# Optimization experiments

Measured on AMD Instinct MI355X. Metric: run time of the kernel, lower is better.

Reference implementation:

```python
import jax, jax.numpy as jnp
import numpy as np
from jax import lax


def setup_inputs() -> dict:
    key = jax.random.key(0)
    ks = jax.random.split(key, 3)
    N, Cin, Cout, H, W = 4, 256, 256, 96, 96
    x = jax.random.normal(ks[0], (N, Cin, H, W), jnp.float32)
    # DCNv2-style internal offset/mask conv: 27 = 9 dy + 9 dx + 9 mask logits
    w_off = jax.random.normal(ks[1], (27, Cin, 3, 3), jnp.float32) * 0.01
    b_off = jnp.zeros((27,), jnp.float32)
    w = jax.random.normal(ks[2], (Cout, Cin, 3, 3), jnp.float32) * (1.0 / np.sqrt(Cin * 9))
    b = jnp.zeros((Cout,), jnp.float32)
    gamma = jnp.ones((Cout,), jnp.float32)
    beta = jnp.zeros((Cout,), jnp.float32)
    return {"x": x, "w_off": w_off, "b_off": b_off, "w": w, "b": b, "gamma": gamma, "beta": beta}


def _bilinear(img, py, px):
    # img: [C,H,W]; py,px: [K,H,W] float sampling coords. Zero outside bounds.
    C, H, W = img.shape
    flat = img.reshape(C, -1)
    y0 = jnp.floor(py)
    x0 = jnp.floor(px)
    ly = py - y0
    lx = px - x0

    def gather(yc, xc):
        valid = (yc >= 0) & (yc <= H - 1) & (xc >= 0) & (xc <= W - 1)
        yi = jnp.clip(yc, 0, H - 1).astype(jnp.int32)
        xi = jnp.clip(xc, 0, W - 1).astype(jnp.int32)
        idx = (yi * W + xi).reshape(-1)
        v = flat[:, idx].reshape((C,) + yc.shape)  # [C,K,H,W]
        return v * valid.astype(img.dtype)

    v00 = gather(y0, x0)
    v01 = gather(y0, x0 + 1)
    v10 = gather(y0 + 1, x0)
    v11 = gather(y0 + 1, x0 + 1)
    return (v00 * (1 - ly) * (1 - lx) + v01 * (1 - ly) * lx
            + v10 * ly * (1 - lx) + v11 * ly * lx)


def _forward(x, w_off, b_off, w, b, gamma, beta):
    N, C, H, W = x.shape
    Cout = w.shape[0]
    dn = ("NCHW", "OIHW", "NCHW")
    # internal offset/mask conv (3x3, stride 1, pad 1)
    om = lax.conv_general_dilated(x, w_off, (1, 1), [(1, 1), (1, 1)], dimension_numbers=dn)
    om = om + b_off[None, :, None, None]
    dy, dx, m = om[:, :9], om[:, 9:18], jax.nn.sigmoid(om[:, 18:])
    # base 3x3 kernel grid, dilation 1, padding 1 (centered taps -1..1)
    ky, kx = jnp.meshgrid(jnp.arange(3) - 1, jnp.arange(3) - 1, indexing="ij")
    py = dy + jnp.arange(H, dtype=x.dtype)[None, None, :, None] + ky.reshape(1, 9, 1, 1).astype(x.dtype)
    px = dx + jnp.arange(W, dtype=x.dtype)[None, None, None, :] + kx.reshape(1, 9, 1, 1).astype(x.dtype)
    sampled = jax.vmap(_bilinear)(x, py, px)  # [N,C,9,H,W]
    sampled = sampled * m[:, None]            # DCNv2 modulation mask
    y = jnp.einsum("nckhw,ock->nohw", sampled, w.reshape(Cout, C, 9))
    y = y + b[None, :, None, None]
    # BatchNorm2d (training-mode batch statistics) + ReLU
    mean = y.mean(axis=(0, 2, 3))
    var = y.var(axis=(0, 2, 3))
    y = (y - mean[None, :, None, None]) * lax.rsqrt(var[None, :, None, None] + 1e-5)
    y = y * gamma[None, :, None, None] + beta[None, :, None, None]
    return jax.nn.relu(y)


def reference(x, w_off, b_off, w, b, gamma, beta):
    return _forward(x, w_off, b_off, w, b, gamma, beta)
```

## Files before the change

kernel.cpp:

```cpp
#include <hip/hip_runtime.h>
#include <cmath>

#define H 96
#define W 96
#define HW 9216
#define CIN 256
#define COUT 256
#define NB 4
#define NCH 72
#define NGR 36
#define NIV 18

typedef float f32x4 __attribute__((ext_vector_type(4)));
typedef float f32x2 __attribute__((ext_vector_type(2)));
typedef short bf16x8 __attribute__((ext_vector_type(8)));

__device__ __forceinline__ unsigned short f2bf(float f) {
  unsigned int u = __float_as_uint(f);
  u += 0x7fff + ((u >> 16) & 1);
  return (unsigned short)(u >> 16);
}
__device__ __forceinline__ float bf2f(unsigned short u) {
  return __uint_as_float(((unsigned int)u) << 16);
}
__device__ __forceinline__ f32x2 up2(unsigned int u) {
  f32x2 r;
  r.x = __uint_as_float(u << 16);
  r.y = __uint_as_float(u & 0xffff0000u);
  return r;
}
__device__ __forceinline__ unsigned int cvtpk(float lo, float hi) {
  unsigned int r;
  asm("v_cvt_pk_bf16_f32 %0, %1, %2" : "=v"(r) : "v"(lo), "v"(hi));
  return r;
}

__device__ __forceinline__ void bar() {
  asm volatile("s_waitcnt lgkmcnt(0)" ::: "memory");
  __builtin_amdgcn_s_barrier();
  asm volatile("" ::: "memory");
}

__global__ __launch_bounds__(256)
void xt_convert(const float* __restrict__ x, unsigned short* __restrict__ xT) {
  __shared__ unsigned short ls[64][72];
  int tid = threadIdx.x;
  int hwbase = blockIdx.x * 64;
  int cbase  = blockIdx.y * 64;
  int n      = blockIdx.z;

  {
    int cl = tid >> 2, qd = tid & 3;
    const float* src = x + ((size_t)(n * CIN + cbase + cl)) * HW + hwbase + qd * 16;
#pragma unroll
    for (int m = 0; m < 4; ++m) {
      float4 v = *(const float4*)(src + m * 4);
      int hwl = qd * 16 + m * 4;
      ls[hwl + 0][cl] = f2bf(v.x);
      ls[hwl + 1][cl] = f2bf(v.y);
      ls[hwl + 2][cl] = f2bf(v.z);
      ls[hwl + 3][cl] = f2bf(v.w);
    }
  }
  __syncthreads();
  {
    int hw = tid >> 2, part = tid & 3;
    unsigned short* dst = xT + ((size_t)(n * HW + hwbase + hw)) * CIN + cbase + part * 16;
    *(uint4*)(dst + 0) = *(const uint4*)(&ls[hw][part * 16 + 0]);
    *(uint4*)(dst + 8) = *(const uint4*)(&ls[hw][part * 16 + 8]);
  }
}

__global__ __launch_bounds__(256)
void wa_all(const float* __restrict__ w, const float* __restrict__ w_off,
            unsigned short* __restrict__ Ag, unsigned short* __restrict__ Ag2,
            float* __restrict__ sumArr) {
  int bx = blockIdx.x;
  int tid = threadIdx.x;
  if (bx < 288) {
    int gid = bx * 256 + tid;
    int ch = gid >> 10;
    int rest = gid & 1023;
    int ot = rest >> 6, l = rest & 63;
    int o = ot * 16 + (l & 15);
    int k = ch >> 3, cc = ch & 7;
    int cbase = cc * 32 + (l >> 4) * 8;
    unsigned short r[8];
#pragma unroll
    for (int j = 0; j < 8; ++j)
      r[j] = f2bf(w[((size_t)o * CIN + cbase + j) * 9 + k]);
    uint4 pk;
    pk.x = (unsigned int)r[0] | ((unsigned int)r[1] << 16);
    pk.y = (unsigned int)r[2] | ((unsigned int)r[3] << 16);
    pk.z = (unsigned int)r[4] | ((unsigned int)r[5] << 16);
    pk.w = (unsigned int)r[6] | ((unsigned int)r[7] << 16);
    *(uint4*)(Ag + (size_t)gid * 8) = pk;
  } else if (bx < 324) {
    int gid = (bx - 288) * 256 + tid;
    int ch = gid >> 7;
    int rest = gid & 127;
    int ot = rest >> 6, l = rest & 63;
    int o = ot * 16 + (l & 15);
    int k = ch >> 3, cc = ch & 7;
    int cbase = cc * 32 + (l >> 4) * 8;
    unsigned short r[8];
#pragma unroll
    for (int j = 0; j < 8; ++j)
      r[j] = (o < 27) ? f2bf(w_off[((size_t)o * CIN + cbase + j) * 9 + k]) : (unsigned short)0;
    uint4 pk;
    pk.x = (unsigned int)r[0] | ((unsigned int)r[1] << 16);
    pk.y = (unsigned int)r[2] | ((unsigned int)r[3] << 16);
    pk.z = (unsigned int)r[4] | ((unsigned int)r[5] << 16);
    pk.w = (unsigned int)r[6] | ((unsigned int)r[7] << 16);
    *(uint4*)(Ag2 + (size_t)gid * 8) = pk;
  } else {
    sumArr[tid] = 0.f;
    sumArr[256 + tid] = 0.f;
  }
}

__global__ __launch_bounds__(512, 4)
void merged_gemm(const unsigned short* __restrict__ xT,
                 const unsigned short* __restrict__ Ag,
                 const unsigned short* __restrict__ Ag2,
                 const float* __restrict__ b_off,
                 unsigned short* __restrict__ yb,
                 float* __restrict__ sumArr, float* __restrict__ sqArr) {
  __shared__ int   sPos[9][64];
  __shared__ float pymk[27][64];
  __shared__ int   sIdx4[9][64][4];
  __shared__ float sWgt4[9][64][4];
  __shared__ unsigned short sB[2][2][4096];

  int tid = threadIdx.x;
  int wv = tid >> 6, lane = tid & 63, quad = lane >> 4, l16 = lane & 15;
  int pixBase = blockIdx.x * 64;
  int n = blockIdx.y;
  const unsigned short* xTn = xT + (size_t)n * HW * CIN;

  if (tid < 64) {
    int hwp = pixBase + tid;
    int hh = hwp / W, wx = hwp % W;
#pragma unroll
    for (int ty = 0; ty < 3; ++ty) {
#pragma unroll
      for (int tx = 0; tx < 3; ++tx) {
        int iy = hh + ty - 1, ix = wx + tx - 1;
        bool ok = (iy >= 0) && (iy < H) && (ix >= 0) && (ix < W);
        sPos[ty * 3 + tx][tid] = ok ? (iy * W + ix) : -1;
      }
    }
  }
  bar();

  int pixA = tid >> 3, ckA = tid & 7;
  int aA = (ckA >> 2) * 2048 + (pixA >> 4) * 512 + ((ckA & 3) * 16 + ((pixA & 15) ^ (ckA & 3))) * 8;

  f32x4 accA[2];
  accA[0] = (f32x4){0.f, 0.f, 0.f, 0.f};
  accA[1] = (f32x4){0.f, 0.f, 0.f, 0.f};

  uint4 dA, dB;
  auto issueA = [&](int g, uint4* d) {
    int k = g % 9, c2 = g / 9;
    int p = sPos[k][pixA];
    *d = (uint4){0, 0, 0, 0};
    if (p >= 0) *d = *(const uint4*)(xTn + (size_t)p * CIN + c2 * 64 + ckA * 8);
  };

  bf16x8 afrA[4];
  auto aloadA = [&](int g) {
    int k = g % 9, c2 = g / 9;
    int ch = k * 8 + c2 * 2;
#pragma unroll
    for (int s = 0; s < 2; ++s)
#pragma unroll
      for (int ot = 0; ot < 2; ++ot)
        afrA[s * 2 + ot] = *(const bf16x8*)(Ag2 + ((size_t)((ch + s) * 2 + ot) * 64 + lane) * 8);
  };

  int rdA = wv * 512 + (quad * 16 + (l16 ^ quad)) * 8;
  auto mfmaA = [&](int buf, int half) {
    const unsigned short* base = &sB[buf][half][0];
    __builtin_amdgcn_s_setprio(1);
#pragma unroll
    for (int s = 0; s < 2; ++s) {
      bf16x8 bfr = *(const bf16x8*)(base + s * 2048 + rdA);
      accA[0] = __builtin_amdgcn_mfma_f32_16x16x32_bf16(afrA[s * 2 + 0], bfr, accA[0], 0, 0, 0);
      accA[1] = __builtin_amdgcn_mfma_f32_16x16x32_bf16(afrA[s * 2 + 1], bfr, accA[1], 0, 0, 0);
    }
    __builtin_amdgcn_s_setprio(0);
  };
  auto storeA = [&](uint4 d, int buf, int half) {
    *(uint4*)(&sB[buf][half][aA]) = d;
  };

  issueA(0, &dA);
  issueA(1, &dB);
  if (wv < 4) aloadA(0);
  storeA(dA, 0, 0);
  issueA(2, &dA);
  storeA(dB, 0, 1);
  issueA(3, &dB);
  bar();

  for (int i = 0; i < NIV; ++i) {
    int buf = i & 1;
    if (wv < 4) {
      mfmaA(buf, 0);
      aloadA(2 * i + 1);
    }
    if (i < NIV - 1) storeA(dA, buf ^ 1, 0);
    if (i < NIV - 2) issueA(2 * i + 4, &dA);
    if (wv < 4) mfmaA(buf, 1);
    if (i < NIV - 1) storeA(dB, buf ^ 1, 1);
    if (i < NIV - 2) issueA(2 * i + 5, &dB);
    if (i < NIV - 1 && wv < 4) aloadA(2 * i + 2);
    bar();
  }

  if (wv < 4) {
    int pixL = wv * 16 + l16;
    int pixG = pixBase + pixL;
    int he = pixG / W, we = pixG % W;
#pragma unroll
    for (int ot = 0; ot < 2; ++ot) {
#pragma unroll
      for (int r = 0; r < 4; ++r) {
        int kk = ot * 16 + quad * 4 + r;
        if (kk >= 27) continue;
        float v = accA[ot][r] + b_off[kk];
        if (kk < 9) {
          pymk[kk][pixL] = v + (float)he + (float)(kk / 3 - 1);
        } else if (kk < 18) {
          int j = kk - 9;
          pymk[kk][pixL] = v + (float)we + (float)(j % 3 - 1);
        } else {
          pymk[kk][pixL] = 1.f / (1.f + expf(-v));
        }
      }
    }
  }
  bar();

  {
    int pix0 = tid & 63;
    int k0 = tid >> 6;
#pragma unroll
    for (int rep = 0; rep < 2; ++rep) {
      int k = (rep == 0) ? k0 : 8;
      if (rep == 1 && tid >= 64) break;
      float fy = pymk[k][pix0], fx = pymk[9 + k][pix0], fm = pymk[18 + k][pix0];
      float y0f = floorf(fy), x0f = floorf(fx);
      float ly = fy - y0f, lx = fx - x0f;
      int y0 = (int)y0f, x0 = (int)x0f;
      int cy0 = min(max(y0, 0), H - 1), cy1 = min(max(y0 + 1, 0), H - 1);
      int cx0 = min(max(x0, 0), W - 1), cx1 = min(max(x0 + 1, 0), W - 1);
      float vy0 = (y0 >= 0 && y0 <= H - 1) ? 1.f : 0.f;
      float vy1 = (y0 + 1 >= 0 && y0 + 1 <= H - 1) ? 1.f : 0.f;
      float vx0 = (x0 >= 0 && x0 <= W - 1) ? 1.f : 0.f;
      float vx1 = (x0 + 1 >= 0 && x0 + 1 <= W - 1) ? 1.f : 0.f;
      int4 iv;
      iv.x = cy0 * W + cx0;
      iv.y = cy0 * W + cx1;
      iv.z = cy1 * W + cx0;
      iv.w = cy1 * W + cx1;
      float4 wf;
      wf.x = (1.f - ly) * (1.f - lx) * fm * vy0 * vx0;
      wf.y = (1.f - ly) * lx * fm * vy0 * vx1;
      wf.z = ly * (1.f - lx) * fm * vy1 * vx0;
      wf.w = ly * lx * fm * vy1 * vx1;
      *(int4*)(&sIdx4[k][pix0][0]) = iv;
      *(float4*)(&sWgt4[k][pix0][0]) = wf;
    }
  }
  bar();

  int pixS  = ((wv & 3) << 4) | (lane >> 2);
  int qS    = lane & 3;
  int chunk = ((wv >> 2) << 2) | qS;
  int co    = chunk * 8;
  int sAddr = (chunk >> 2) * 2048 + (wv & 3) * 512 + (qS * 16 + ((lane >> 2) ^ qS)) * 8;

  f32x4 acc[2][4];
#pragma unroll
  for (int i = 0; i < 2; ++i)
#pragma unroll
    for (int pt = 0; pt < 4; ++pt) acc[i][pt] = (f32x4){0.f, 0.f, 0.f, 0.f};

  uint4 cnA[4], cnB[4];
  float wgA[4], wgB[4];
  auto issue = [&](int g, uint4* cn, float* wt) {
    int k = g % 9, c2 = g / 9;
    int4 iv = *(const int4*)(&sIdx4[k][pixS][0]);
    float4 wf = *(const float4*)(&sWgt4[k][pixS][0]);
    int coff = c2 * 64 + co;
    cn[0] = *(const uint4*)(xTn + (size_t)iv.x * CIN + coff);
    cn[1] = *(const uint4*)(xTn + (size_t)iv.y * CIN + coff);
    cn[2] = *(const uint4*)(xTn + (size_t)iv.z * CIN + coff);
    cn[3] = *(const uint4*)(xTn + (size_t)iv.w * CIN + coff);
    wt[0] = wf.x; wt[1] = wf.y; wt[2] = wf.z; wt[3] = wf.w;
  };

  auto blendOne = [&](unsigned int u0, unsigned int u1, unsigned int u2,
                      unsigned int u3, const float* wt) -> unsigned int {
    f32x2 s = up2(u0) * wt[0];
    s += up2(u1) * wt[1];
    s += up2(u2) * wt[2];
    s += up2(u3) * wt[3];
    return cvtpk(s.x, s.y);
  };
  auto blendStore = [&](uint4* cn, const float* wt, int buf, int half) {
    uint4 r;
    r.x = blendOne(cn[0].x, cn[1].x, cn[2].x, cn[3].x, wt);
    r.y = blendOne(cn[0].y, cn[1].y, cn[2].y, cn[3].y, wt);
    r.z = blendOne(cn[0].z, cn[1].z, cn[2].z, cn[3].z, wt);
    r.w = blendOne(cn[0].w, cn[1].w, cn[2].w, cn[3].w, wt);
    *(uint4*)(&sB[buf][half][sAddr]) = r;
  };

  bf16x8 afr[4];
  auto aload = [&](int g) {
    int k = g % 9, c2 = g / 9;
    int ch = k * 8 + c2 * 2;
#pragma unroll
    for (int s = 0; s < 2; ++s)
#pragma unroll
      for (int ot = 0; ot < 2; ++ot)
        afr[s * 2 + ot] = *(const bf16x8*)(Ag + ((size_t)((ch + s) * 16 + 2 * wv + ot) * 64 + lane) * 8);
  };

  int rdBase = (quad * 16 + (l16 ^ quad)) * 8;
  auto mfmaPhase = [&](int buf, int half) {
    const unsigned short* base = &sB[buf][half][0];
    __builtin_amdgcn_s_setprio(1);
#pragma unroll
    for (int s = 0; s < 2; ++s) {
      bf16x8 bfr[4];
#pragma unroll
      for (int pt = 0; pt < 4; ++pt)
        bfr[pt] = *(const bf16x8*)(base + s * 2048 + pt * 512 + rdBase);
#pragma unroll
      for (int pt = 0; pt < 4; ++pt) {
        acc[0][pt] = __builtin_amdgcn_mfma_f32_16x16x32_bf16(afr[s * 2 + 0], bfr[pt], acc[0][pt], 0, 0, 0);
        acc[1][pt] = __builtin_amdgcn_mfma_f32_16x16x32_bf16(afr[s * 2 + 1], bfr[pt], acc[1][pt], 0, 0, 0);
      }
    }
    __builtin_amdgcn_s_setprio(0);
  };

  issue(0, cnA, wgA);
  issue(1, cnB, wgB);
  aload(0);
  blendStore(cnA, wgA, 0, 0);
  issue(2, cnA, wgA);
  blendStore(cnB, wgB, 0, 1);
  issue(3, cnB, wgB);
  bar();

  for (int i = 0; i < NIV; ++i) {
    int buf = i & 1;
    mfmaPhase(buf, 0);
    aload(2 * i + 1);
    if (i < NIV - 1) blendStore(cnA, wgA, buf ^ 1, 0);
    if (i < NIV - 2) issue(2 * i + 4, cnA, wgA);
    mfmaPhase(buf, 1);
    if (i < NIV - 1) blendStore(cnB, wgB, buf ^ 1, 1);
    if (i < NIV - 2) issue(2 * i + 5, cnB, wgB);
    if (i < NIV - 1) aload(2 * i + 2);
    bar();
  }

#pragma unroll
  for (int ot = 0; ot < 2; ++ot) {
#pragma unroll
    for (int r = 0; r < 4; ++r) {
      int o = (2 * wv + ot) * 16 + quad * 4 + r;
      unsigned short* rowp = yb + (size_t)(n * COUT + o) * HW + pixBase;
      float s = 0.f, q = 0.f;
#pragma unroll
      for (int pt = 0; pt < 4; ++pt) {
        float v = acc[ot][pt][r];
        rowp[pt * 16 + l16] = f2bf(v);
        s += v;
        q = fmaf(v, v, q);
      }
#pragma unroll
      for (int m = 8; m >= 1; m >>= 1) {
        s += __shfl_xor(s, m, 64);
        q += __shfl_xor(q, m, 64);
      }
      if (l16 == 0) {
        atomicAdd(&sumArr[o], s);
        atomicAdd(&sqArr[o], q);
      }
    }
  }
}

__global__ __launch_bounds__(256)
void bn_apply(const unsigned short* __restrict__ yb,
              float* __restrict__ out,
              const float* __restrict__ sumArr,
              const float* __restrict__ sqArr,
              const float* __restrict__ gamma,
              const float* __restrict__ beta) {
  int gid = blockIdx.x * 256 + threadIdx.x;
  int base = gid * 8;
  int o = (base / HW) % COUT;
  const float inv = 1.f / (float)(NB * HW);
  float mean = sumArr[o] * inv;
  float var = sqArr[o] * inv - mean * mean;
  float scale = rsqrtf(var + 1e-5f) * gamma[o];
  float shift = beta[o] - mean * scale;
  uint4 v = ((const uint4*)yb)[gid];
  float4 a, b;
  a.x = fmaxf(fmaf(bf2f((unsigned short)(v.x & 0xffff)), scale, shift), 0.f);
  a.y = fmaxf(fmaf(bf2f((unsigned short)(v.x >> 16)), scale, shift), 0.f);
  a.z = fmaxf(fmaf(bf2f((unsigned short)(v.y & 0xffff)), scale, shift), 0.f);
  a.w = fmaxf(fmaf(bf2f((unsigned short)(v.y >> 16)), scale, shift), 0.f);
  b.x = fmaxf(fmaf(bf2f((unsigned short)(v.z & 0xffff)), scale, shift), 0.f);
  b.y = fmaxf(fmaf(bf2f((unsigned short)(v.z >> 16)), scale, shift), 0.f);
  b.z = fmaxf(fmaf(bf2f((unsigned short)(v.w & 0xffff)), scale, shift), 0.f);
  b.w = fmaxf(fmaf(bf2f((unsigned short)(v.w >> 16)), scale, shift), 0.f);
  *(float4*)&out[base] = a;
  *(float4*)&out[base + 4] = b;
}

extern "C" void kernel_launch(void* const* d_in, const int* in_sizes, int n_in,
                              void* d_out, int out_size, void* d_ws, size_t ws_size,
                              hipStream_t stream) {
  const float* x     = (const float*)d_in[0];
  const float* w_off = (const float*)d_in[1];
  const float* b_off = (const float*)d_in[2];
  const float* w     = (const float*)d_in[3];
  const float* gamma = (const float*)d_in[5];
  const float* beta  = (const float*)d_in[6];
  float* out = (float*)d_out;

  unsigned short* Ag  = (unsigned short*)d_ws;
  unsigned short* Ag2 = Ag + 589824;
  float* sumArr   = (float*)(Ag2 + 73728);
  float* sqArr    = sumArr + 256;
  unsigned short* yb = (unsigned short*)(sqArr + 256);
  unsigned short* xT = yb + 9437184;

  dim3 gT(HW / 64, CIN / 64, NB);
  xt_convert<<<gT, 256, 0, stream>>>(x, xT);

  wa_all<<<325, 256, 0, stream>>>(w, w_off, Ag, Ag2, sumArr);

  dim3 gM(HW / 64, NB);
  merged_gemm<<<gM, 512, 0, stream>>>(xT, Ag, Ag2, b_off, yb, sumArr, sqArr);

  bn_apply<<<(NB * COUT * HW / 8) / 256, 256, 0, stream>>>(yb, out, sumArr, sqArr, gamma, beta);
}
```

Baseline: 259.6 us.

## Recompute sampling indices and weights inline to cut LDS and raise occupancy

Removes the shared-memory tables for 3x3 neighbour positions and the bilinear corner indices/weights. These are now recomputed per issue from pixel coordinates and the raw offset/mask values in pymk. This drops two barriers and frees roughly 20 KB of LDS per block, and the launch bound is raised to 8 blocks per CU. The trade-off is extra ALU work in the gather loop and tighter register limits, which may cause spills.

New measurement: 844.6 us. +225.3%, slower.

```diff
diff --git a/kernel.cpp b/kernel.cpp
--- a/kernel.cpp
+++ b/kernel.cpp
@@ -119,17 +119,14 @@
   }
 }
 
-__global__ __launch_bounds__(512, 4)
+__global__ __launch_bounds__(512, 8)
 void merged_gemm(const unsigned short* __restrict__ xT,
                  const unsigned short* __restrict__ Ag,
                  const unsigned short* __restrict__ Ag2,
                  const float* __restrict__ b_off,
                  unsigned short* __restrict__ yb,
                  float* __restrict__ sumArr, float* __restrict__ sqArr) {
-  __shared__ int   sPos[9][64];
   __shared__ float pymk[27][64];
-  __shared__ int   sIdx4[9][64][4];
-  __shared__ float sWgt4[9][64][4];
   __shared__ unsigned short sB[2][2][4096];
 
   int tid = threadIdx.x;
@@ -138,22 +135,9 @@
   int n = blockIdx.y;
   const unsigned short* xTn = xT + (size_t)n * HW * CIN;
 
-  if (tid < 64) {
-    int hwp = pixBase + tid;
-    int hh = hwp / W, wx = hwp % W;
-#pragma unroll
-    for (int ty = 0; ty < 3; ++ty) {
-#pragma unroll
-      for (int tx = 0; tx < 3; ++tx) {
-        int iy = hh + ty - 1, ix = wx + tx - 1;
-        bool ok = (iy >= 0) && (iy < H) && (ix >= 0) && (ix < W);
-        sPos[ty * 3 + tx][tid] = ok ? (iy * W + ix) : -1;
-      }
-    }
-  }
-  bar();
-
   int pixA = tid >> 3, ckA = tid & 7;
+  int hwpA = pixBase + pixA;
+  int hhA = hwpA / W, wxA = hwpA % W;
   int aA = (ckA >> 2) * 2048 + (pixA >> 4) * 512 + ((ckA & 3) * 16 + ((pixA & 15) ^ (ckA & 3))) * 8;
 
   f32x4 accA[2];
@@ -163,9 +147,12 @@
   uint4 dA, dB;
   auto issueA = [&](int g, uint4* d) {
     int k = g % 9, c2 = g / 9;
-    int p = sPos[k][pixA];
+    int ty = (k * 171) >> 9;
+    int tx = k - ty * 3;
+    int iy = hhA + ty - 1, ix = wxA + tx - 1;
+    bool ok = (iy >= 0) && (iy < H) && (ix >= 0) && (ix < W);
     *d = (uint4){0, 0, 0, 0};
-    if (p >= 0) *d = *(const uint4*)(xTn + (size_t)p * CIN + c2 * 64 + ckA * 8);
+    if (ok) *d = *(const uint4*)(xTn + (size_t)(iy * W + ix) * CIN + c2 * 64 + ckA * 8);
   };
 
   bf16x8 afrA[4];
@@ -243,39 +230,6 @@
   }
   bar();
 
-  {
-    int pix0 = tid & 63;
-    int k0 = tid >> 6;
-#pragma unroll
-    for (int rep = 0; rep < 2; ++rep) {
-      int k = (rep == 0) ? k0 : 8;
-      if (rep == 1 && tid >= 64) break;
-      float fy = pymk[k][pix0], fx = pymk[9 + k][pix0], fm = pymk[18 + k][pix0];
-      float y0f = floorf(fy), x0f = floorf(fx);
-      float ly = fy - y0f, lx = fx - x0f;
-      int y0 = (int)y0f, x0 = (int)x0f;
-      int cy0 = min(max(y0, 0), H - 1), cy1 = min(max(y0 + 1, 0), H - 1);
-      int cx0 = min(max(x0, 0), W - 1), cx1 = min(max(x0 + 1, 0), W - 1);
-      float vy0 = (y0 >= 0 && y0 <= H - 1) ? 1.f : 0.f;
-      float vy1 = (y0 + 1 >= 0 && y0 + 1 <= H - 1) ? 1.f : 0.f;
-      float vx0 = (x0 >= 0 && x0 <= W - 1) ? 1.f : 0.f;
-      float vx1 = (x0 + 1 >= 0 && x0 + 1 <= W - 1) ? 1.f : 0.f;
-      int4 iv;
-      iv.x = cy0 * W + cx0;
-      iv.y = cy0 * W + cx1;
-      iv.z = cy1 * W + cx0;
-      iv.w = cy1 * W + cx1;
-      float4 wf;
-      wf.x = (1.f - ly) * (1.f - lx) * fm * vy0 * vx0;
-      wf.y = (1.f - ly) * lx * fm * vy0 * vx1;
-      wf.z = ly * (1.f - lx) * fm * vy1 * vx0;
-      wf.w = ly * lx * fm * vy1 * vx1;
-      *(int4*)(&sIdx4[k][pix0][0]) = iv;
-      *(float4*)(&sWgt4[k][pix0][0]) = wf;
-    }
-  }
-  bar();
-
   int pixS  = ((wv & 3) << 4) | (lane >> 2);
   int qS    = lane & 3;
   int chunk = ((wv >> 2) << 2) | qS;
@@ -292,14 +246,25 @@
   float wgA[4], wgB[4];
   auto issue = [&](int g, uint4* cn, float* wt) {
     int k = g % 9, c2 = g / 9;
-    int4 iv = *(const int4*)(&sIdx4[k][pixS][0]);
-    float4 wf = *(const float4*)(&sWgt4[k][pixS][0]);
+    float fy = pymk[k][pixS], fx = pymk[9 + k][pixS], fm = pymk[18 + k][pixS];
+    float y0f = floorf(fy), x0f = floorf(fx);
+    float ly = fy - y0f, lx = fx - x0f;
+    int y0 = (int)y0f, x0 = (int)x0f;
+    int cy0 = min(max(y0, 0), H - 1), cy1 = min(max(y0 + 1, 0), H - 1);
+    int cx0 = min(max(x0, 0), W - 1), cx1 = min(max(x0 + 1, 0), W - 1);
+    float vy0 = (y0 >= 0 && y0 <= H - 1) ? 1.f : 0.f;
+    float vy1 = (y0 + 1 >= 0 && y0 + 1 <= H - 1) ? 1.f : 0.f;
+    float vx0 = (x0 >= 0 && x0 <= W - 1) ? 1.f : 0.f;
+    float vx1 = (x0 + 1 >= 0 && x0 + 1 <= W - 1) ? 1.f : 0.f;
     int coff = c2 * 64 + co;
-    cn[0] = *(const uint4*)(xTn + (size_t)iv.x * CIN + coff);
-    cn[1] = *(const uint4*)(xTn + (size_t)iv.y * CIN + coff);
-    cn[2] = *(const uint4*)(xTn + (size_t)iv.z * CIN + coff);
-    cn[3] = *(const uint4*)(xTn + (size_t)iv.w * CIN + coff);
-    wt[0] = wf.x; wt[1] = wf.y; wt[2] = wf.z; wt[3] = wf.w;
+    cn[0] = *(const uint4*)(xTn + (size_t)(cy0 * W + cx0) * CIN + coff);
+    cn[1] = *(const uint4*)(xTn + (size_t)(cy0 * W + cx1) * CIN + coff);
+    cn[2] = *(const uint4*)(xTn + (size_t)(cy1 * W + cx0) * CIN + coff);
+    cn[3] = *(const uint4*)(xTn + (size_t)(cy1 * W + cx1) * CIN + coff);
+    wt[0] = (1.f - ly) * (1.f - lx) * fm * vy0 * vx0;
+    wt[1] = (1.f - ly) * lx * fm * vy0 * vx1;
+    wt[2] = ly * (1.f - lx) * fm * vy1 * vx0;
+    wt[3] = ly * lx * fm * vy1 * vx1;
   };
 
   auto blendOne = [&](unsigned int u0, unsigned int u1, unsigned int u2,
```
